# Kernel tuning notes

Hardware: AMD Instinct MI355X
Metric: run time of the kernel (lower is better)

Reference implementation:

```python
import jax, jax.numpy as jnp
import numpy as np

HEADS = 16
D_HID = 64
N_EMBED = HEADS * D_HID  # 1024; also must equal k_len for the final out @ v


def setup_inputs() -> dict:
    key = jax.random.key(0)
    kq, kk, kv, km = jax.random.split(key, 4)
    B, QL, KL = 4, 2048, 1024
    q = jax.random.normal(kq, (B, QL, N_EMBED), dtype=jnp.float32)
    k = jax.random.normal(kk, (B, KL, N_EMBED), dtype=jnp.float32)
    v = jax.random.normal(kv, (B, KL, N_EMBED), dtype=jnp.float32)
    mask = jax.random.randint(km, (B, QL, 1, KL), 0, 2, dtype=jnp.int32)
    return {"q": q, "k": k, "v": v, "mask": mask}


def reference(q, k, v, mask):
    B, QL, E = q.shape
    KL = k.shape[1]
    H, D = HEADS, D_HID
    qh = q.reshape(B, QL, H, D)
    kh = k.reshape(B, KL, H, D)
    vh = v.reshape(B, KL, H, D)
    # energy: (B, q, h, k), softmax over key axis (dim=3 in the original)
    energy = jnp.einsum('nqhd,nkhd->nqhk', qh, kh)
    energy = jnp.where(mask == 0, jnp.float32(-1e20), energy)
    attention = jax.nn.softmax(energy / jnp.sqrt(jnp.float32(E)), axis=3)
    out = jnp.einsum('nqhk,nkhd->nqhd', attention, vh).reshape(B, QL, H * D)
    # second softmax over the model dim (self.softmax = nn.Softmax(dim=-1))
    out = jax.nn.softmax(out, axis=-1)
    # out @ v : (B, QL, E) @ (B, KL==E, E) -> (B, QL, E)
    v2 = jnp.matmul(out, v)
    return (v2, out)
```

## Files before the change

### kernel.cpp

```cpp
#include <hip/hip_runtime.h>
#include <hip/hip_bf16.h>
#include <stdint.h>

#define HEADS 16
#define DH 64
#define NE 1024
#define BB 4
#define QL 2048
#define KLEN 1024

typedef __attribute__((ext_vector_type(8))) short bf16x8;
typedef __attribute__((ext_vector_type(4))) float f32x4;
typedef unsigned short u16;
typedef unsigned int u32;
typedef unsigned long long u64;

__device__ __forceinline__ u16 f2b(float f){
  union { float f; unsigned u; } v; v.f = f;
  unsigned r = v.u + 0x7fffu + ((v.u >> 16) & 1u);
  return (u16)(r >> 16);
}
__device__ __forceinline__ u32 pack2(float a, float b){
  return (u32)f2b(a) | ((u32)f2b(b) << 16);
}
__device__ __forceinline__ u32 cvtpk(float a, float b){
  u32 r; asm("v_cvt_pk_bf16_f32 %0, %1, %2" : "=v"(r) : "v"(a), "v"(b)); return r;
}
__device__ __forceinline__ void gload16(const void* g, void* l){
  __builtin_amdgcn_global_load_lds((const __attribute__((address_space(1))) u32*)g,
                                   (__attribute__((address_space(3))) u32*)l, 16, 0, 0);
}

__global__ __launch_bounds__(256) void kpack_kernel(const float* __restrict__ k,
    u16* __restrict__ kp){
  int id = blockIdx.x * 256 + threadIdx.x;
  int u = id & 511, kt = (id >> 9) & 15, h = (id >> 13) & 15, b = id >> 17;
  int row = u >> 3, blk = u & 7, d0 = ((blk ^ (row & 7)) << 3);
  const float* src = k + ((size_t)(b * KLEN + kt * 64 + row)) * NE + h * DH + d0;
  float4 f0 = *(const float4*)src;
  float4 f1 = *(const float4*)(src + 4);
  uint4 o;
  o.x = pack2(f0.x, f0.y); o.y = pack2(f0.z, f0.w);
  o.z = pack2(f1.x, f1.y); o.w = pack2(f1.z, f1.w);
  ((uint4*)kp)[id] = o;
}

__global__ __launch_bounds__(256) void vpack_kernel(const float* __restrict__ v,
    u16* __restrict__ vp){
  __shared__ __attribute__((aligned(16))) u16 t[64][72];
  const int b = blockIdx.z, h = blockIdx.y, kt = blockIdx.x;
  const int tid = threadIdx.x;
  {
    int key = tid >> 2, dseg = (tid & 3) * 16;
    const float* src = v + ((size_t)(b * KLEN + kt * 64 + key)) * NE + h * DH + dseg;
#pragma unroll
    for (int i = 0; i < 16; i += 4){
      float4 f = *(const float4*)(src + i);
      t[dseg + i + 0][key] = f2b(f.x); t[dseg + i + 1][key] = f2b(f.y);
      t[dseg + i + 2][key] = f2b(f.z); t[dseg + i + 3][key] = f2b(f.w);
    }
  }
  __syncthreads();
  {
    int row = tid >> 2, p2 = (tid & 3) * 2;
    u16* dst = vp + ((size_t)((b * HEADS + h) * 16 + kt)) * 4096;
#pragma unroll
    for (int e = 0; e < 2; e++){
      int blk = p2 + e, sb = blk ^ (row & 7);
      uint4 d4 = *(const uint4*)&t[row][sb * 8];
      *(uint4*)(dst + (row * 8 + blk) * 8) = d4;
    }
  }
}

__global__ __launch_bounds__(256) void mbits_kernel(const int* __restrict__ mask,
    u64* __restrict__ mb){
  int t = blockIdx.x * 256 + threadIdx.x;
  u64 bal = __ballot(mask[t] != 0);
  if ((threadIdx.x & 63) == 0) mb[t >> 6] = bal;
}

__global__ __launch_bounds__(256) void attn1_kernel(
    const float* __restrict__ q, const u16* __restrict__ kp,
    const u16* __restrict__ vp, const u64* __restrict__ mb,
    float* __restrict__ out1){
  __shared__ __attribute__((aligned(16))) u16 Kt[2][4096];
  __shared__ __attribute__((aligned(16))) u16 Vt[2][4096];
  __shared__ __attribute__((aligned(16))) u16 Pt[4][2][16][72];
  __shared__ u64 LUT[16];
  const int b = blockIdx.z, h = blockIdx.y, q0 = blockIdx.x * 128;
  const int tid = threadIdx.x, w = tid >> 6, l = tid & 63;
  const int lq = l & 15, g = l >> 4;
  const int qrowA = q0 + w * 32 + lq;
  const int qrowB = qrowA + 16;
  const float C2 = 0.0450842200278f;

  if (tid < 16){
    u32 n = tid;
    u32 m0 = (n & 1 ? 0xFFFFu : 0u) | (n & 2 ? 0xFFFF0000u : 0u);
    u32 m1 = (n & 4 ? 0xFFFFu : 0u) | (n & 8 ? 0xFFFF0000u : 0u);
    LUT[n] = (u64)m0 | ((u64)m1 << 32);
  }

  bf16x8 bqA0, bqA1, bqB0, bqB1;
#define LOADQ(D0, D1, QROW) {                                                  \
    const float* qsrc = q + ((size_t)b * QL + (QROW)) * NE + h * DH + g * 8;   \
    float4 f0 = *(const float4*)(qsrc);                                        \
    float4 f1 = *(const float4*)(qsrc + 4);                                    \
    float4 f2 = *(const float4*)(qsrc + 32);                                   \
    float4 f3 = *(const float4*)(qsrc + 36);                                   \
    D0[0]=(short)f2b(f0.x*C2); D0[1]=(short)f2b(f0.y*C2);                      \
    D0[2]=(short)f2b(f0.z*C2); D0[3]=(short)f2b(f0.w*C2);                      \
    D0[4]=(short)f2b(f1.x*C2); D0[5]=(short)f2b(f1.y*C2);                      \
    D0[6]=(short)f2b(f1.z*C2); D0[7]=(short)f2b(f1.w*C2);                      \
    D1[0]=(short)f2b(f2.x*C2); D1[1]=(short)f2b(f2.y*C2);                      \
    D1[2]=(short)f2b(f2.z*C2); D1[3]=(short)f2b(f2.w*C2);                      \
    D1[4]=(short)f2b(f3.x*C2); D1[5]=(short)f2b(f3.y*C2);                      \
    D1[6]=(short)f2b(f3.z*C2); D1[7]=(short)f2b(f3.w*C2); }
  LOADQ(bqA0, bqA1, qrowA)
  LOADQ(bqB0, bqB1, qrowB)
#undef LOADQ

  const f32x4 fz = {0.f, 0.f, 0.f, 0.f};
  f32x4 accOA[4], accOB[4];
#pragma unroll
  for (int t2 = 0; t2 < 4; t2++){ accOA[t2] = fz; accOB[t2] = fz; }
  f32x4 accLA = fz, accLB = fz;
  const short one_bf = (short)0x3F80;
  const bf16x8 ones = {one_bf, one_bf, one_bf, one_bf, one_bf, one_bf, one_bf, one_bf};

  const u64* mrowA = mb + ((size_t)b * QL + qrowA) * (KLEN / 64);
  const u64* mrowB = mb + ((size_t)b * QL + qrowB) * (KLEN / 64);
  const u16* kT0 = kp + ((size_t)((b * HEADS + h) * 16)) * 4096;
  const u16* vT0 = vp + ((size_t)((b * HEADS + h) * 16)) * 4096;
  const int blkA = g ^ (lq & 7);
  const int bK0 = lq * 128 + blkA * 16;
  const int bK1 = lq * 128 + (blkA ^ 4) * 16;
  char* KtC = (char*)Kt;
  char* VtC = (char*)Vt;

  gload16(kT0 + (size_t)tid * 8,         KtC + w * 1024);
  gload16(kT0 + (size_t)(256 + tid) * 8, KtC + 4096 + w * 1024);
  gload16(vT0 + (size_t)tid * 8,         VtC + w * 1024);
  gload16(vT0 + (size_t)(256 + tid) * 8, VtC + 4096 + w * 1024);

  int cur = 0;
  for (int kt = 0; kt < 16; ++kt){
    __syncthreads();
    if (kt < 15){
      const u16* ksn = kT0 + (size_t)(kt + 1) * 4096;
      const u16* vsn = vT0 + (size_t)(kt + 1) * 4096;
      char* Kd = KtC + (cur ^ 1) * 8192;
      char* Vd = VtC + (cur ^ 1) * 8192;
      gload16(ksn + (size_t)tid * 8,         Kd + w * 1024);
      gload16(ksn + (size_t)(256 + tid) * 8, Kd + 4096 + w * 1024);
      gload16(vsn + (size_t)tid * 8,         Vd + w * 1024);
      gload16(vsn + (size_t)(256 + tid) * 8, Vd + 4096 + w * 1024);
    }
    u64 mwA = mrowA[kt], mwB = mrowB[kt];
    const char* Kb = KtC + cur * 8192;
    const char* Vb = VtC + cur * 8192;

    f32x4 sA[4], sB[4];
#pragma unroll
    for (int c = 0; c < 4; c++){ sA[c] = fz; sB[c] = fz; }
#pragma unroll
    for (int c = 0; c < 4; c++){
      bf16x8 a0 = *(const bf16x8*)(Kb + bK0 + c * 2048);
      bf16x8 a1 = *(const bf16x8*)(Kb + bK1 + c * 2048);
      sA[c] = __builtin_amdgcn_mfma_f32_16x16x32_bf16(a0, bqA0, sA[c], 0, 0, 0);
      sA[c] = __builtin_amdgcn_mfma_f32_16x16x32_bf16(a1, bqA1, sA[c], 0, 0, 0);
      sB[c] = __builtin_amdgcn_mfma_f32_16x16x32_bf16(a0, bqB0, sB[c], 0, 0, 0);
      sB[c] = __builtin_amdgcn_mfma_f32_16x16x32_bf16(a1, bqB1, sB[c], 0, 0, 0);
    }

#define SOFTMAX_SUB(SV, MW, SUB, AP0, AP1, ACCL)                               \
    {                                                                          \
      u32 pw[8];                                                               \
      _Pragma("unroll") for (int c = 0; c < 4; c++){                           \
        float p0 = __builtin_amdgcn_exp2f(SV[c][0]);                           \
        float p1 = __builtin_amdgcn_exp2f(SV[c][1]);                           \
        float p2 = __builtin_amdgcn_exp2f(SV[c][2]);                           \
        float p3 = __builtin_amdgcn_exp2f(SV[c][3]);                           \
        pw[2 * c]     = cvtpk(p0, p1);                                         \
        pw[2 * c + 1] = cvtpk(p2, p3);                                         \
      }                                                                        \
      {                                                                        \
        u32 mwlo = (u32)(MW), mwhi = (u32)((MW) >> 32);                        \
        int s0_ = 4 * g;                                                       \
        u64 M0 = LUT[(mwlo >> s0_) & 0xFu];                                    \
        u64 M1 = LUT[(mwlo >> (s0_ + 16)) & 0xFu];                             \
        u64 M2 = LUT[(mwhi >> s0_) & 0xFu];                                    \
        u64 M3 = LUT[(mwhi >> (s0_ + 16)) & 0xFu];                             \
        pw[0] &= (u32)M0; pw[1] &= (u32)(M0 >> 32);                            \
        pw[2] &= (u32)M1; pw[3] &= (u32)(M1 >> 32);                            \
        pw[4] &= (u32)M2; pw[5] &= (u32)(M2 >> 32);                            \
        pw[6] &= (u32)M3; pw[7] &= (u32)(M3 >> 32);                            \
      }                                                                        \
      _Pragma("unroll") for (int c = 0; c < 4; c++){                           \
        uint2 u2; u2.x = pw[2 * c]; u2.y = pw[2 * c + 1];                      \
        *(uint2*)&Pt[w][SUB][lq][16 * c + 4 * g] = u2;                         \
      }                                                                        \
      asm volatile("" ::: "memory");                                           \
      AP0 = *(const bf16x8*)&Pt[w][SUB][lq][g * 8];                            \
      AP1 = *(const bf16x8*)&Pt[w][SUB][lq][32 + g * 8];                       \
      ACCL = __builtin_amdgcn_mfma_f32_16x16x32_bf16(AP0, ones, ACCL, 0, 0, 0);\
      ACCL = __builtin_amdgcn_mfma_f32_16x16x32_bf16(AP1, ones, ACCL, 0, 0, 0);\
    }

    bf16x8 apA0, apA1, apB0, apB1;
    SOFTMAX_SUB(sA, mwA, 0, apA0, apA1, accLA)
    SOFTMAX_SUB(sB, mwB, 1, apB0, apB1, accLB)
#undef SOFTMAX_SUB

#pragma unroll
    for (int t2 = 0; t2 < 4; t2++){
      bf16x8 bv0 = *(const bf16x8*)(Vb + bK0 + t2 * 2048);
      bf16x8 bv1 = *(const bf16x8*)(Vb + bK1 + t2 * 2048);
      accOA[t2] = __builtin_amdgcn_mfma_f32_16x16x32_bf16(apA0, bv0, accOA[t2], 0, 0, 0);
      accOA[t2] = __builtin_amdgcn_mfma_f32_16x16x32_bf16(apA1, bv1, accOA[t2], 0, 0, 0);
      accOB[t2] = __builtin_amdgcn_mfma_f32_16x16x32_bf16(apB0, bv0, accOB[t2], 0, 0, 0);
      accOB[t2] = __builtin_amdgcn_mfma_f32_16x16x32_bf16(apB1, bv1, accOB[t2], 0, 0, 0);
    }
    cur ^= 1;
  }

  float liA0 = 1.f / accLA[0], liA1 = 1.f / accLA[1];
  float liA2 = 1.f / accLA[2], liA3 = 1.f / accLA[3];
  float liB0 = 1.f / accLB[0], liB1 = 1.f / accLB[1];
  float liB2 = 1.f / accLB[2], liB3 = 1.f / accLB[3];
  float* opA = out1 + ((size_t)b * QL + q0 + w * 32) * NE + h * DH;
  float* opB = opA + (size_t)16 * NE;
#pragma unroll
  for (int t2 = 0; t2 < 4; t2++){
    opA[(4*g+0) * NE + t2 * 16 + lq] = accOA[t2][0] * liA0;
    opA[(4*g+1) * NE + t2 * 16 + lq] = accOA[t2][1] * liA1;
    opA[(4*g+2) * NE + t2 * 16 + lq] = accOA[t2][2] * liA2;
    opA[(4*g+3) * NE + t2 * 16 + lq] = accOA[t2][3] * liA3;
    opB[(4*g+0) * NE + t2 * 16 + lq] = accOB[t2][0] * liB0;
    opB[(4*g+1) * NE + t2 * 16 + lq] = accOB[t2][1] * liB1;
    opB[(4*g+2) * NE + t2 * 16 + lq] = accOB[t2][2] * liB2;
    opB[(4*g+3) * NE + t2 * 16 + lq] = accOB[t2][3] * liB3;
  }
}

__global__ __launch_bounds__(256) void softmax2_kernel(float* __restrict__ o,
    u16* __restrict__ wp){
  const int row = blockIdx.x, tid = threadIdx.x;
  float* p = o + (size_t)row * NE + tid * 4;
  float4 x = *(const float4*)p;
  float mx = fmaxf(fmaxf(x.x, x.y), fmaxf(x.z, x.w));
#pragma unroll
  for (int off = 32; off >= 1; off >>= 1) mx = fmaxf(mx, __shfl_xor(mx, off, 64));
  __shared__ float red[8];
  const int wv = tid >> 6;
  if ((tid & 63) == 0) red[wv] = mx;
  __syncthreads();
  mx = fmaxf(fmaxf(red[0], red[1]), fmaxf(red[2], red[3]));
  float e0 = __expf(x.x - mx), e1 = __expf(x.y - mx);
  float e2 = __expf(x.z - mx), e3 = __expf(x.w - mx);
  float s = (e0 + e1) + (e2 + e3);
#pragma unroll
  for (int off = 32; off >= 1; off >>= 1) s += __shfl_xor(s, off, 64);
  if ((tid & 63) == 0) red[4 + wv] = s;
  __syncthreads();
  s = (red[4] + red[5]) + (red[6] + red[7]);
  float inv = 1.f / s;
  x.x = e0 * inv; x.y = e1 * inv; x.z = e2 * inv; x.w = e3 * inv;
  *(float4*)p = x;
  if (wp){
    int b = row >> 11, qi = row & 2047;
    int qt = qi >> 6, rw = qi & 63;
    int ktile = tid >> 4, db = (tid >> 1) & 7, half = tid & 1;
    size_t tile = (size_t)((b * 32 + qt) * 16 + ktile);
    char* dst = (char*)wp + tile * 8192 + rw * 128 + ((db ^ (rw & 7)) * 16) + half * 8;
    uint2 u2; u2.x = cvtpk(x.x, x.y); u2.y = cvtpk(x.z, x.w);
    *(uint2*)dst = u2;
  }
}

__global__ __launch_bounds__(256) void gemm3f_kernel(const u16* __restrict__ wp,
    const u16* __restrict__ vp, float* __restrict__ v2){
  __shared__ __attribute__((aligned(16))) u16 Wt[2][4096];
  __shared__ __attribute__((aligned(16))) u16 Vt3[2][4096];
  const int b = blockIdx.z, qt = blockIdx.y, h3 = blockIdx.x;
  const int tid = threadIdx.x, w = tid >> 6, l = tid & 63;
  const int lq = l & 15, g = l >> 4;
  const int blkA = g ^ (lq & 7);
  const int bK0 = lq * 128 + blkA * 16;
  const int bK1 = lq * 128 + (blkA ^ 4) * 16;
  char* WtC = (char*)Wt;
  char* VtC = (char*)Vt3;
  const f32x4 fz = {0.f, 0.f, 0.f, 0.f};
  f32x4 acc[4];
#pragma unroll
  for (int t2 = 0; t2 < 4; t2++) acc[t2] = fz;
  const u16* wT0 = wp + ((size_t)((b * 32 + qt) * 16)) * 4096;
  const u16* vT0 = vp + ((size_t)((b * HEADS + h3) * 16)) * 4096;

  gload16(wT0 + (size_t)tid * 8,         WtC + w * 1024);
  gload16(wT0 + (size_t)(256 + tid) * 8, WtC + 4096 + w * 1024);
  gload16(vT0 + (size_t)tid * 8,         VtC + w * 1024);
  gload16(vT0 + (size_t)(256 + tid) * 8, VtC + 4096 + w * 1024);

  int cur = 0;
  for (int ksv = 0; ksv < 16; ++ksv){
    __syncthreads();
    if (ksv < 15){
      const u16* wsn = wT0 + (size_t)(ksv + 1) * 4096;
      const u16* vsn = vT0 + (size_t)(ksv + 1) * 4096;
      char* Wd = WtC + (cur ^ 1) * 8192;
      char* Vd = VtC + (cur ^ 1) * 8192;
      gload16(wsn + (size_t)tid * 8,         Wd + w * 1024);
      gload16(wsn + (size_t)(256 + tid) * 8, Wd + 4096 + w * 1024);
      gload16(vsn + (size_t)tid * 8,         Vd + w * 1024);
      gload16(vsn + (size_t)(256 + tid) * 8, Vd + 4096 + w * 1024);
    }
    const char* Wb = WtC + cur * 8192;
    const char* Vb = VtC + cur * 8192;
    bf16x8 a0 = *(const bf16x8*)(Wb + w * 2048 + bK0);
    bf16x8 a1 = *(const bf16x8*)(Wb + w * 2048 + bK1);
#pragma unroll
    for (int t2 = 0; t2 < 4; t2++){
      bf16x8 b0 = *(const bf16x8*)(Vb + bK0 + t2 * 2048);
      bf16x8 b1 = *(const bf16x8*)(Vb + bK1 + t2 * 2048);
      acc[t2] = __builtin_amdgcn_mfma_f32_16x16x32_bf16(a0, b0, acc[t2], 0, 0, 0);
      acc[t2] = __builtin_amdgcn_mfma_f32_16x16x32_bf16(a1, b1, acc[t2], 0, 0, 0);
    }
    cur ^= 1;
  }
  float* op = v2 + ((size_t)b * QL + qt * 64 + w * 16) * NE + h3 * 64;
#pragma unroll
  for (int t2 = 0; t2 < 4; t2++){
#pragma unroll
    for (int r = 0; r < 4; r++){
      op[(4 * g + r) * NE + t2 * 16 + lq] = acc[t2][r];
    }
  }
}

__global__ __launch_bounds__(256) void gemm3_kernel(const float* __restrict__ w2,
    const u16* __restrict__ vp, float* __restrict__ v2){
  __shared__ __attribute__((aligned(16))) u16 Wt[4096];
  __shared__ __attribute__((aligned(16))) u16 Vt3[4096];
  const int b = blockIdx.z, q0 = blockIdx.y * 64, n0 = blockIdx.x * 64;
  const int tid = threadIdx.x, w = tid >> 6, l = tid & 63;
  const int lq = l & 15, g = l >> 4;
  const int blkA = g ^ (lq & 7);
  const int bK0 = lq * 128 + blkA * 16;
  const int bK1 = lq * 128 + (blkA ^ 4) * 16;
  char* WtC = (char*)Wt;
  char* VtC = (char*)Vt3;
  const f32x4 fz = {0.f, 0.f, 0.f, 0.f};
  f32x4 acc[4];
#pragma unroll
  for (int t2 = 0; t2 < 4; t2++) acc[t2] = fz;
  const float* wsrc0 = w2 + ((size_t)b * QL + q0) * NE;
  const u16* vT0 = vp + ((size_t)((b * HEADS + (n0 >> 6)) * 16)) * 4096;
  const int rr = tid >> 4, cc = tid & 15;

  for (int ksv = 0; ksv < 16; ++ksv){
    __syncthreads();
#pragma unroll
    for (int pp = 0; pp < 4; pp++){
      int r2 = pp * 16 + rr;
      float4 f = *(const float4*)(wsrc0 + (size_t)r2 * NE + ksv * 64 + cc * 4);
      int blkL = (cc >> 1) ^ (r2 & 7);
      uint2 u2; u2.x = cvtpk(f.x, f.y); u2.y = cvtpk(f.z, f.w);
      *(uint2*)(WtC + (r2 * 8 + blkL) * 16 + (cc & 1) * 8) = u2;
    }
    const u16* vs = vT0 + ksv * 4096;
    gload16(vs + (size_t)tid * 8,         VtC + w * 1024);
    gload16(vs + (size_t)(256 + tid) * 8, VtC + 4096 + w * 1024);
    __syncthreads();
    bf16x8 a0 = *(const bf16x8*)(WtC + w * 2048 + bK0);
    bf16x8 a1 = *(const bf16x8*)(WtC + w * 2048 + bK1);
#pragma unroll
    for (int t2 = 0; t2 < 4; t2++){
      bf16x8 b0 = *(const bf16x8*)(VtC + bK0 + t2 * 2048);
      bf16x8 b1 = *(const bf16x8*)(VtC + bK1 + t2 * 2048);
      acc[t2] = __builtin_amdgcn_mfma_f32_16x16x32_bf16(a0, b0, acc[t2], 0, 0, 0);
      acc[t2] = __builtin_amdgcn_mfma_f32_16x16x32_bf16(a1, b1, acc[t2], 0, 0, 0);
    }
  }
  float* op = v2 + ((size_t)b * QL + q0 + w * 16) * NE + n0;
#pragma unroll
  for (int t2 = 0; t2 < 4; t2++){
#pragma unroll
    for (int r = 0; r < 4; r++){
      op[(4 * g + r) * NE + t2 * 16 + lq] = acc[t2][r];
    }
  }
}

extern "C" void kernel_launch(void* const* d_in, const int* in_sizes, int n_in,
                              void* d_out, int out_size, void* d_ws, size_t ws_size,
                              hipStream_t stream){
  const float* q = (const float*)d_in[0];
  const float* k = (const float*)d_in[1];
  const float* v = (const float*)d_in[2];
  const int* mask = (const int*)d_in[3];
  float* v2 = (float*)d_out;
  float* out2 = v2 + (size_t)BB * QL * NE;

  char* wsb = (char*)d_ws;
  u16* kp  = (u16*)wsb;
  u16* vpk = (u16*)(wsb + (8u << 20));
  u64* mbp = (u64*)(wsb + (16u << 20));
  u16* wpk = (u16*)(wsb + (17u << 20));
  const bool fast = ws_size >= (34ull << 20);

  kpack_kernel<<<2048, 256, 0, stream>>>(k, kp);
  vpack_kernel<<<dim3(16, HEADS, BB), 256, 0, stream>>>(v, vpk);
  mbits_kernel<<<BB * QL * KLEN / 256, 256, 0, stream>>>(mask, mbp);
  attn1_kernel<<<dim3(QL / 128, HEADS, BB), 256, 0, stream>>>(q, kp, vpk, mbp, out2);
  softmax2_kernel<<<BB * QL, 256, 0, stream>>>(out2, fast ? wpk : (u16*)nullptr);
  if (fast){
    gemm3f_kernel<<<dim3(NE / 64, QL / 64, BB), 256, 0, stream>>>(wpk, vpk, v2);
  } else {
    gemm3_kernel<<<dim3(NE / 64, QL / 64, BB), 256, 0, stream>>>(out2, vpk, v2);
  }
}
```

Measured before the change: 140.0 us.

## Keep softmax probabilities in registers by transposing the PV MFMA operand order

```diff
diff --git a/kernel.cpp b/kernel.cpp
--- a/kernel.cpp
+++ b/kernel.cpp
@@ -86,7 +86,6 @@
     float* __restrict__ out1){
   __shared__ __attribute__((aligned(16))) u16 Kt[2][4096];
   __shared__ __attribute__((aligned(16))) u16 Vt[2][4096];
-  __shared__ __attribute__((aligned(16))) u16 Pt[4][2][16][72];
   __shared__ u64 LUT[16];
   const int b = blockIdx.z, h = blockIdx.y, q0 = blockIdx.x * 128;
   const int tid = threadIdx.x, w = tid >> 6, l = tid & 63;
@@ -174,7 +173,7 @@
       sB[c] = __builtin_amdgcn_mfma_f32_16x16x32_bf16(a1, bqB1, sB[c], 0, 0, 0);
     }
 
-#define SOFTMAX_SUB(SV, MW, SUB, AP0, AP1, ACCL)                               \
+#define SOFTMAX_SUB(SV, MW, PB0, PB1, ACCL)                                    \
     {                                                                          \
       u32 pw[8];                                                               \
       _Pragma("unroll") for (int c = 0; c < 4; c++){                           \
@@ -197,50 +196,57 @@
         pw[4] &= (u32)M2; pw[5] &= (u32)(M2 >> 32);                            \
         pw[6] &= (u32)M3; pw[7] &= (u32)(M3 >> 32);                            \
       }                                                                        \
-      _Pragma("unroll") for (int c = 0; c < 4; c++){                           \
-        uint2 u2; u2.x = pw[2 * c]; u2.y = pw[2 * c + 1];                      \
-        *(uint2*)&Pt[w][SUB][lq][16 * c + 4 * g] = u2;                         \
-      }                                                                        \
-      asm volatile("" ::: "memory");                                           \
-      AP0 = *(const bf16x8*)&Pt[w][SUB][lq][g * 8];                            \
-      AP1 = *(const bf16x8*)&Pt[w][SUB][lq][32 + g * 8];                       \
-      ACCL = __builtin_amdgcn_mfma_f32_16x16x32_bf16(AP0, ones, ACCL, 0, 0, 0);\
-      ACCL = __builtin_amdgcn_mfma_f32_16x16x32_bf16(AP1, ones, ACCL, 0, 0, 0);\
-    }
-
-    bf16x8 apA0, apA1, apB0, apB1;
-    SOFTMAX_SUB(sA, mwA, 0, apA0, apA1, accLA)
-    SOFTMAX_SUB(sB, mwB, 1, apB0, apB1, accLB)
+      PB0.u4.x = pw[0]; PB0.u4.y = pw[1]; PB0.u4.z = pw[2]; PB0.u4.w = pw[3];  \
+      PB1.u4.x = pw[4]; PB1.u4.y = pw[5]; PB1.u4.z = pw[6]; PB1.u4.w = pw[7];  \
+      ACCL = __builtin_amdgcn_mfma_f32_16x16x32_bf16(ones, PB0.v8, ACCL, 0, 0, 0);\
+      ACCL = __builtin_amdgcn_mfma_f32_16x16x32_bf16(ones, PB1.v8, ACCL, 0, 0, 0);\
+    }
+
+    union bfu { uint4 u4; bf16x8 v8; };
+    bfu pbA0, pbA1, pbB0, pbB1;
+    SOFTMAX_SUB(sA, mwA, pbA0, pbA1, accLA)
+    SOFTMAX_SUB(sB, mwB, pbB0, pbB1, accLB)
 #undef SOFTMAX_SUB
 
-#pragma unroll
-    for (int t2 = 0; t2 < 4; t2++){
-      bf16x8 bv0 = *(const bf16x8*)(Vb + bK0 + t2 * 2048);
-      bf16x8 bv1 = *(const bf16x8*)(Vb + bK1 + t2 * 2048);
-      accOA[t2] = __builtin_amdgcn_mfma_f32_16x16x32_bf16(apA0, bv0, accOA[t2], 0, 0, 0);
-      accOA[t2] = __builtin_amdgcn_mfma_f32_16x16x32_bf16(apA1, bv1, accOA[t2], 0, 0, 0);
-      accOB[t2] = __builtin_amdgcn_mfma_f32_16x16x32_bf16(apB0, bv0, accOB[t2], 0, 0, 0);
-      accOB[t2] = __builtin_amdgcn_mfma_f32_16x16x32_bf16(apB1, bv1, accOB[t2], 0, 0, 0);
+    {
+      const int gOff = (g & 1) * 8;
+      const int gHi = g >> 1;
+#pragma unroll
+      for (int t2 = 0; t2 < 4; t2++){
+        const char* vrow = Vb + (t2 * 16 + lq) * 128;
+        const int rx = lq & 7;
+        bfu va0, va1;
+        {
+          uint2 lo_ = *(const uint2*)(vrow + (((0 + gHi) ^ rx) << 4) + gOff);
+          uint2 hi_ = *(const uint2*)(vrow + (((2 + gHi) ^ rx) << 4) + gOff);
+          va0.u4.x = lo_.x; va0.u4.y = lo_.y; va0.u4.z = hi_.x; va0.u4.w = hi_.y;
+        }
+        {
+          uint2 lo_ = *(const uint2*)(vrow + (((4 + gHi) ^ rx) << 4) + gOff);
+          uint2 hi_ = *(const uint2*)(vrow + (((6 + gHi) ^ rx) << 4) + gOff);
+          va1.u4.x = lo_.x; va1.u4.y = lo_.y; va1.u4.z = hi_.x; va1.u4.w = hi_.y;
+        }
+        accOA[t2] = __builtin_amdgcn_mfma_f32_16x16x32_bf16(va0.v8, pbA0.v8, accOA[t2], 0, 0, 0);
+        accOA[t2] = __builtin_amdgcn_mfma_f32_16x16x32_bf16(va1.v8, pbA1.v8, accOA[t2], 0, 0, 0);
+        accOB[t2] = __builtin_amdgcn_mfma_f32_16x16x32_bf16(va0.v8, pbB0.v8, accOB[t2], 0, 0, 0);
+        accOB[t2] = __builtin_amdgcn_mfma_f32_16x16x32_bf16(va1.v8, pbB1.v8, accOB[t2], 0, 0, 0);
+      }
     }
     cur ^= 1;
   }
 
-  float liA0 = 1.f / accLA[0], liA1 = 1.f / accLA[1];
-  float liA2 = 1.f / accLA[2], liA3 = 1.f / accLA[3];
-  float liB0 = 1.f / accLB[0], liB1 = 1.f / accLB[1];
-  float liB2 = 1.f / accLB[2], liB3 = 1.f / accLB[3];
-  float* opA = out1 + ((size_t)b * QL + q0 + w * 32) * NE + h * DH;
-  float* opB = opA + (size_t)16 * NE;
+  float liA = 1.f / accLA[0];
+  float liB = 1.f / accLB[0];
+  float* opA = out1 + ((size_t)b * QL + qrowA) * NE + h * DH + 4 * g;
+  float* opB = out1 + ((size_t)b * QL + qrowB) * NE + h * DH + 4 * g;
 #pragma unroll
   for (int t2 = 0; t2 < 4; t2++){
-    opA[(4*g+0) * NE + t2 * 16 + lq] = accOA[t2][0] * liA0;
-    opA[(4*g+1) * NE + t2 * 16 + lq] = accOA[t2][1] * liA1;
-    opA[(4*g+2) * NE + t2 * 16 + lq] = accOA[t2][2] * liA2;
-    opA[(4*g+3) * NE + t2 * 16 + lq] = accOA[t2][3] * liA3;
-    opB[(4*g+0) * NE + t2 * 16 + lq] = accOB[t2][0] * liB0;
-    opB[(4*g+1) * NE + t2 * 16 + lq] = accOB[t2][1] * liB1;
-    opB[(4*g+2) * NE + t2 * 16 + lq] = accOB[t2][2] * liB2;
-    opB[(4*g+3) * NE + t2 * 16 + lq] = accOB[t2][3] * liB3;
+    float4 stA = {accOA[t2][0] * liA, accOA[t2][1] * liA,
+                  accOA[t2][2] * liA, accOA[t2][3] * liA};
+    float4 stB = {accOB[t2][0] * liB, accOB[t2][1] * liB,
+                  accOB[t2][2] * liB, accOB[t2][3] * liB};
+    *(float4*)(opA + t2 * 16) = stA;
+    *(float4*)(opB + t2 * 16) = stB;
   }
 }
 
```

Result: slower. 142.8 us (+2.0%).
